# Kernel tuning notes

Measured on AMD Instinct MI355X. Metric: run time of the kernel, lower is better.

## Reference

```python
import jax, jax.numpy as jnp
import numpy as np

NUM_GRAPHS = 1024
EPS = 1e-5  # BatchNorm eps
NEG_SLOPE = 0.2  # GATConv leaky_relu slope


def _bn(x, g, b):
    # train-mode BatchNorm over node/graph axis (biased variance, as torch)
    mu = jnp.mean(x, axis=0)
    var = jnp.mean((x - mu) ** 2, axis=0)
    return (x - mu) * jax.lax.rsqrt(var + EPS) * g + b


def _prelu(x, a):
    return jnp.where(x > 0, x, a * x)


def _gat_layer(x, src, dst, W, a_src, a_dst, bias, n_nodes):
    # single-head GATConv (heads=1, concat=True), self-loops already in src/dst
    h = x @ W                                            # [N, C]
    e = jax.nn.leaky_relu(jnp.take(h @ a_src, src) + jnp.take(h @ a_dst, dst), NEG_SLOPE)  # [E]
    m = jax.ops.segment_max(e, dst, num_segments=n_nodes)
    ex = jnp.exp(e - jnp.take(m, dst))
    denom = jax.ops.segment_sum(ex, dst, num_segments=n_nodes)
    alpha = ex / (jnp.take(denom, dst) + 1e-16)          # softmax over in-edges of each target
    out = jax.ops.segment_sum(jnp.take(h, src, axis=0) * alpha[:, None], dst, num_segments=n_nodes)
    return out + bias


def setup_inputs() -> dict:
    key = jax.random.key(0)
    ks = jax.random.split(key, 16)
    N, E, F, H, C = 500_000, 8_000_000, 7, 8, 2

    def gl(k, shp, fan_in):
        return (jax.random.normal(k, shp, jnp.float32) / np.sqrt(fan_in)).astype(jnp.float32)

    return {
        "x": jax.random.normal(ks[0], (N, F), jnp.float32),
        "edge_index": jax.random.randint(ks[1], (2, E), 0, N, jnp.int32),
        "batch": jnp.sort(jax.random.randint(ks[2], (N,), 0, NUM_GRAPHS, jnp.int32)),
        "W1": gl(ks[3], (F, H), F), "as1": gl(ks[4], (H,), H), "ad1": gl(ks[5], (H,), H), "b1": jnp.zeros((H,), jnp.float32),
        "W2": gl(ks[6], (H, H), H), "as2": gl(ks[7], (H,), H), "ad2": gl(ks[8], (H,), H), "b2": jnp.zeros((H,), jnp.float32),
        "W3": gl(ks[9], (H, H), H), "as3": gl(ks[10], (H,), H), "ad3": gl(ks[11], (H,), H), "b3": jnp.zeros((H,), jnp.float32),
        "g1": jnp.ones((H,), jnp.float32), "be1": jnp.zeros((H,), jnp.float32),
        "g2": jnp.ones((H,), jnp.float32), "be2": jnp.zeros((H,), jnp.float32),
        "g3": jnp.ones((H,), jnp.float32), "be3": jnp.zeros((H,), jnp.float32),
        "a_gnn": jnp.float32(0.25),
        "Wjk": gl(ks[12], (3 * H, H), 3 * H), "bjk": jnp.zeros((H,), jnp.float32),
        "Wm1": gl(ks[13], (H, H), H), "bm1": jnp.zeros((H,), jnp.float32),
        "gm": jnp.ones((H,), jnp.float32), "bem": jnp.zeros((H,), jnp.float32),
        "a_mlp": jnp.float32(0.25),
        "Wm2": gl(ks[14], (H, C), H), "bm2": jnp.zeros((C,), jnp.float32),
    }


def reference(x, edge_index, batch,
              W1, as1, ad1, b1, W2, as2, ad2, b2, W3, as3, ad3, b3,
              g1, be1, g2, be2, g3, be3, a_gnn, Wjk, bjk,
              Wm1, bm1, gm, bem, a_mlp, Wm2, bm2):
    N = x.shape[0]
    loop = jnp.arange(N, dtype=edge_index.dtype)  # GATConv add_self_loops=True
    src = jnp.concatenate([edge_index[0], loop])
    dst = jnp.concatenate([edge_index[1], loop])
    # 3-layer GAT, each: conv -> BatchNorm -> PReLU (dropout omitted: eval)
    h1 = _prelu(_bn(_gat_layer(x, src, dst, W1, as1, ad1, b1, N), g1, be1), a_gnn)
    h2 = _prelu(_bn(_gat_layer(h1, src, dst, W2, as2, ad2, b2, N), g2, be2), a_gnn)
    h3 = _prelu(_bn(_gat_layer(h2, src, dst, W3, as3, ad3, b3, N), g3, be3), a_gnn)
    # JumpingKnowledge 'cat' + projection to out_channels
    h = jnp.concatenate([h1, h2, h3], axis=1) @ Wjk + bjk   # [N, 8]
    pooled = jax.ops.segment_sum(h, batch, num_segments=NUM_GRAPHS)  # global_add_pool [G, 8]
    m1 = _prelu(_bn(pooled @ Wm1 + bm1, gm, bem), a_mlp)    # MLP hidden
    return m1 @ Wm2 + bm2                                    # [G, 2] logits
```

## Files before the change

### kernel.cpp

```cpp
#include <hip/hip_runtime.h>

typedef unsigned short u16;
typedef unsigned int   u32;

#define EPSBN     1e-5f
#define NEG_SLOPE 0.2f
#define NGRAPH    1024
#define NPB       512
#define CHUNK     16384
#define BKCAP     11264
#define NTILE     8
#define SLOTS     1536


static __device__ __forceinline__ float bfl(const u16* __restrict__ p, int i){
    return __uint_as_float(((u32)p[i]) << 16);
}
static __device__ __forceinline__ float ldf(const void* __restrict__ p, int i, bool f32){
    return f32 ? ((const float*)p)[i] : bfl((const u16*)p, i);
}
static __device__ __forceinline__ u16 f2bf(float f){
    u32 u = __float_as_uint(f);
    return (u16)((u + 0x7fffu + ((u >> 16) & 1u)) >> 16);
}
static __device__ __forceinline__ void unpack8(uint4 pk, float* a){
    a[0] = __uint_as_float((pk.x & 0xffffu) << 16);
    a[1] = __uint_as_float( pk.x & 0xffff0000u);
    a[2] = __uint_as_float((pk.y & 0xffffu) << 16);
    a[3] = __uint_as_float( pk.y & 0xffff0000u);
    a[4] = __uint_as_float((pk.z & 0xffffu) << 16);
    a[5] = __uint_as_float( pk.z & 0xffff0000u);
    a[6] = __uint_as_float((pk.w & 0xffffu) << 16);
    a[7] = __uint_as_float( pk.w & 0xffff0000u);
}
static __device__ __forceinline__ uint4 pack8(const float* a){
    uint4 pk;
    pk.x = (u32)f2bf(a[0]) | ((u32)f2bf(a[1])<<16);
    pk.y = (u32)f2bf(a[2]) | ((u32)f2bf(a[3])<<16);
    pk.z = (u32)f2bf(a[4]) | ((u32)f2bf(a[5])<<16);
    pk.w = (u32)f2bf(a[6]) | ((u32)f2bf(a[7])<<16);
    return pk;
}

static __device__ __forceinline__ int wave_scan_incl(int x){
    int lane = threadIdx.x & 63;
    #pragma unroll
    for (int off = 1; off < 64; off <<= 1){
        int y = __shfl_up(x, off, 64);
        if (lane >= off) x += y;
    }
    return x;
}
static __device__ __forceinline__ int block_scan_incl(int x, int* wpart){
    int t = threadIdx.x, lane = t & 63, wv = t >> 6;
    int nw = blockDim.x >> 6;
    int ws = wave_scan_incl(x);
    __syncthreads();
    if (lane == 63) wpart[wv] = ws;
    __syncthreads();
    if (wv == 0){
        int p = (lane < nw) ? wpart[lane] : 0;
        p = wave_scan_incl(p);
        if (lane < nw) wpart[lane] = p;
    }
    __syncthreads();
    int base = wv ? wpart[wv-1] : 0;
    return base + ws;
}

__global__ void k_sniff(const u16* __restrict__ x, int* __restrict__ flag){
    int lane = threadIdx.x;
    bool hit = false;
    for (int i = lane; i < 128; i += 64){
        float v = bfl(x, i);
        if (!(fabsf(v) <= 1e6f)) hit = true;
    }
    unsigned long long m = __ballot(hit);
    if (lane == 0) flag[0] = (m != 0ull) ? 1 : 0;
}

__global__ __launch_bounds__(1024) void k_binsort(const int* __restrict__ src,
                                                  const int* __restrict__ dst,
                                                  u32* __restrict__ stage,
                                                  int* __restrict__ matL,
                                                  int E, int B){
    __shared__ u32 pr[CHUNK];
    __shared__ int h[2048];
    __shared__ int wpart[16];
    int c = blockIdx.x, t = threadIdx.x;
    int e0 = c << 14, e1 = min(e0 + CHUNK, E), cn = e1 - e0;
    for (int b = t; b < B; b += 1024) h[b] = 0;
    __syncthreads();
    for (int i = e0 + t; i < e1; i += 1024) atomicAdd(&h[dst[i] >> 9], 1);
    __syncthreads();
    int base = t << 1, run = 0, loc[2];
    #pragma unroll
    for (int j = 0; j < 2; j++){
        int b = base + j;
        int v = (b < B) ? h[b] : 0;
        loc[j] = run; run += v;
    }
    int incl = block_scan_incl(run, wpart);
    int bex = incl - run;
    __syncthreads();
    #pragma unroll
    for (int j = 0; j < 2; j++){
        int b = base + j;
        if (b < B) h[b] = bex + loc[j];
    }
    __syncthreads();
    int* mrow = matL + (size_t)c * (B+1);
    for (int b = t; b < B; b += 1024) mrow[b] = h[b];
    if (t == 0) mrow[B] = cn;
    __syncthreads();
    for (int i = e0 + t; i < e1; i += 1024){
        int d = dst[i];
        int b = d >> 9;
        int p = atomicAdd(&h[b], 1);
        pr[p] = ((u32)src[i] << 9) | (u32)(d & 511);
    }
    __syncthreads();
    u32* srow = stage + ((size_t)c << 14);
    for (int i = t; i < cn; i += 1024) srow[i] = pr[i];
}

__global__ __launch_bounds__(256) void k_mtrans(const int* __restrict__ matL,
                                                int* __restrict__ matT, int R, int C){
    __shared__ int tile[32][33];
    int tx = threadIdx.x & 31, ty = threadIdx.x >> 5;
    int c0 = blockIdx.x << 5, r0 = blockIdx.y << 5;
    for (int j = ty; j < 32; j += 8){
        int r = r0 + j, c = c0 + tx;
        if (r < C && c < R) tile[j][tx] = matL[(size_t)r*R + c];
    }
    __syncthreads();
    for (int j = ty; j < 32; j += 8){
        int cc = c0 + j, rr = r0 + tx;
        if (cc < R && rr < C) matT[(size_t)cc*C + rr] = tile[tx][j];
    }
}

__global__ __launch_bounds__(256) void k_bucketsum(const int* __restrict__ matT,
                                                   int* __restrict__ bb, int B, int NC){
    int b = blockIdx.x, t = threadIdx.x;
    __shared__ int s[256];
    int acc = 0;
    const int* r0 = matT + (size_t)b*NC;
    const int* r1 = matT + (size_t)(b+1)*NC;
    for (int c = t; c < NC; c += 256) acc += r1[c] - r0[c];
    s[t] = acc; __syncthreads();
    for (int off = 128; off > 0; off >>= 1){
        if (t < off) s[t] += s[t+off];
        __syncthreads();
    }
    if (t == 0) bb[b] = s[0];
}

__global__ __launch_bounds__(1024) void k_bktbase(int* __restrict__ bb, int B,
                                                  float* __restrict__ statsAll){
    __shared__ int wpart[16];
    int t = threadIdx.x;
    if (t < 48) statsAll[t] = 0.f;
    int v = (t < B) ? bb[t] : 0;
    int incl = block_scan_incl(v, wpart);
    if (t < B) bb[t] = incl - v;
    if (t == B-1) bb[B] = incl;
}

__global__ __launch_bounds__(1024) void k_bucket(const u32* __restrict__ stage,
                                                 const int* __restrict__ matT,
                                                 const int* __restrict__ bb,
                                                 int* __restrict__ tileOfs,
                                                 u32* __restrict__ csr,
                                                 int N, int B, int NC){
    __shared__ u32 pr[BKCAP];
    __shared__ int hist[4096];
    __shared__ int sc[1024];
    __shared__ int lofsA[512];
    __shared__ int wpart[16];
    int k = blockIdx.x, t = threadIdx.x;
    int n0 = k << 9, n1 = min(n0 + NPB, N), nn = n1 - n0;
    int cnt = 0, lofs = 0;
    if (t < NC){
        lofs = matT[(size_t)k*NC + t];
        cnt  = matT[(size_t)(k+1)*NC + t] - lofs;
    }
    if (t < 512) lofsA[t] = lofs;
    int incl1 = block_scan_incl(cnt, wpart);
    sc[t] = incl1;
    __syncthreads();
    int total = sc[1023];
    int ec    = min(total, BKCAP - nn);
    for (int pidx = t; pidx < ec; pidx += 1024){
        int lo = 0, hi = 511;
        while (lo < hi){ int mid = (lo + hi) >> 1; if (sc[mid] > pidx) hi = mid; else lo = mid + 1; }
        int segStart = lo ? sc[lo-1] : 0;
        pr[pidx] = stage[((size_t)lo << 14) + lofsA[lo] + (pidx - segStart)];
    }
    __syncthreads();
    for (int j = t; j < nn; j += 1024) pr[ec + j] = ((u32)(n0 + j) << 9) | (u32)j;
    int ecnt = ec + nn;
    for (int i = t; i < 4096; i += 1024) hist[i] = 0;
    __syncthreads();
    for (int i = t; i < ecnt; i += 1024){
        u32 pk = pr[i];
        int dl = pk & 511;
        int tile = min((int)(pk >> 9) >> 16, NTILE-1);
        atomicAdd(&hist[(tile << 9) + dl], 1);
    }
    __syncthreads();
    int base = t << 2, run = 0, loc[4];
    #pragma unroll
    for (int j = 0; j < 4; j++){ loc[j] = run; run += hist[base + j]; }
    int incl2 = block_scan_incl(run, wpart);
    int bex = incl2 - run;
    __syncthreads();
    #pragma unroll
    for (int j = 0; j < 4; j++) hist[base + j] = bex + loc[j];
    if ((t & 127) == 0) tileOfs[(size_t)k*9 + (t >> 7)] = bex;
    if (t == 0)         tileOfs[(size_t)k*9 + 8] = ecnt;
    __syncthreads();
    int wbase = bb[k] + n0;
    for (int i = t; i < ecnt; i += 1024){
        u32 pk = pr[i];
        int dl = pk & 511;
        int tile = min((int)(pk >> 9) >> 16, NTILE-1);
        int p = atomicAdd(&hist[(tile << 9) + dl], 1);
        csr[wbase + p] = pk;
    }
}

__global__ void k_transform(const uint4* __restrict__ actpk, const void* __restrict__ xraw,
                            const int* __restrict__ dflag, int fin,
                            const void* __restrict__ W, const void* __restrict__ adst,
                            const float* __restrict__ stats, const void* __restrict__ gamma,
                            const void* __restrict__ beta, const void* __restrict__ alpha,
                            uint4* __restrict__ hrec, float* __restrict__ hd, int n){
    const bool f32 = dflag[0] != 0;
    __shared__ float Wl[64], dl[8], scl[8], sft[8], alv;
    int t = threadIdx.x;
    if (t < 64)            Wl[t]   = (t < fin*8) ? ldf(W, t, f32) : 0.f;
    if (t >= 64 && t < 72) dl[t-64] = ldf(adst, t-64, f32);
    if (t == 80) alv = ldf(alpha, 0, f32);
    if (stats && t < 8){
        float invN = 1.f/(float)n;
        float mu  = stats[t]*invN;
        float var = fmaxf(stats[8+t]*invN - mu*mu, 0.f);
        float s   = ldf(gamma, t, f32)*rsqrtf(var + EPSBN);
        scl[t] = s; sft[t] = ldf(beta, t, f32) - mu*s;
    }
    __syncthreads();
    int i = blockIdx.x*blockDim.x + t;
    if (i >= n) return;
    float a[8];
    if (xraw){
        #pragma unroll
        for (int k=0;k<7;k++) a[k] = ldf(xraw, i*7 + k, f32);
        a[7] = 0.f;
    } else {
        unpack8(actpk[i], a);
        #pragma unroll
        for (int j=0;j<8;j++){
            float y = a[j]*scl[j] + sft[j];
            a[j] = (y > 0.f) ? y : alv*y;
        }
    }
    float h[8];
    #pragma unroll
    for (int j=0;j<8;j++){
        float acc = 0.f;
        #pragma unroll
        for (int k=0;k<8;k++) acc += a[k]*Wl[k*8+j];
        h[j] = acc;
    }
    float s2 = 0.f;
    #pragma unroll
    for (int j=0;j<8;j++) s2 += h[j]*dl[j];
    hd[i] = s2;
    hrec[i] = pack8(h);
}

__global__ __launch_bounds__(512) void k_aggregate(
        const u32* __restrict__ csr, const int* __restrict__ bb,
        const int* __restrict__ tileOfs,
        const uint4* __restrict__ hrec, const float* __restrict__ hd,
        const void* __restrict__ asrc, const int* __restrict__ dflag,
        uint4* __restrict__ act, float* __restrict__ stats, int n){
    const bool f32 = dflag[0] != 0;
    __shared__ u32 stg[5*SLOTS];
    __shared__ u16 bs[512], be[512];
    __shared__ float alS[8];
    __shared__ float sred[8][16];
    __shared__ int tofS[9];
    int k = blockIdx.x, t = threadIdx.x;
    int n0 = k << 9;
    int nn = min(NPB, n - n0);
    if (t < 8) alS[t] = ldf(asrc, t, f32);
    if (t < 9) tofS[t] = tileOfs[(size_t)k*9 + t];
    float hdv = (t < nn) ? hd[n0 + t] : 0.f;
    int e0 = bb[k] + n0;
    __syncthreads();
    float al[8];
    #pragma unroll
    for (int j = 0; j < 8; j++) al[j] = alS[j];
    float acc[8] = {0,0,0,0,0,0,0,0};
    float den = 0.f;

    int wt = 0, wc = 0;
    while (wt < NTILE && wc >= tofS[wt+1]){ wt++; if (wt < NTILE) wc = tofS[wt]; }

    u32 pkc[3]; uint4 hvc[3];
    if (wt < NTILE){
        int L = min(SLOTS, tofS[wt+1] - wc);
        #pragma unroll
        for (int j = 0; j < 3; j++) pkc[j] = csr[e0 + wc + min(t + (j << 9), L - 1)];
        #pragma unroll
        for (int j = 0; j < 3; j++) hvc[j] = hrec[pkc[j] >> 9];
    }

    while (wt < NTILE){
        int L = min(SLOTS, tofS[wt+1] - wc);
        __syncthreads();
        #pragma unroll
        for (int j = 0; j < 3; j++){
            int i = t + (j << 9);
            if (i < L){
                stg[0*SLOTS + i] = hvc[j].x;
                stg[1*SLOTS + i] = hvc[j].y;
                stg[2*SLOTS + i] = hvc[j].z;
                stg[3*SLOTS + i] = hvc[j].w;
                stg[4*SLOTS + i] = pkc[j] & 511u;
            }
        }
        bs[t] = 0; be[t] = 0;
        __syncthreads();
        int nwt = wt, nwc = wc + SLOTS;
        while (nwt < NTILE && nwc >= tofS[nwt+1]){ nwt++; if (nwt < NTILE) nwc = tofS[nwt]; }
        if (nwt < NTILE){
            int Ln = min(SLOTS, tofS[nwt+1] - nwc);
            #pragma unroll
            for (int j = 0; j < 3; j++) pkc[j] = csr[e0 + nwc + min(t + (j << 9), Ln - 1)];
            #pragma unroll
            for (int j = 0; j < 3; j++) hvc[j] = hrec[pkc[j] >> 9];
        }
        for (int i = t; i < L; i += 512){
            int dl = (int)stg[4*SLOTS + i];
            if (i == 0){
                bs[dl] = 0;
            } else {
                int dp = (int)stg[4*SLOTS + i - 1];
                if (dp != dl){ bs[dl] = (u16)i; be[dp] = (u16)i; }
            }
            if (i == L-1) be[dl] = (u16)L;
        }
        __syncthreads();
        {
            int p0 = bs[t], p1 = be[t];
            for (int p = p0; p < p1; ++p){
                uint4 hv = make_uint4(stg[0*SLOTS + p], stg[1*SLOTS + p],
                                      stg[2*SLOTS + p], stg[3*SLOTS + p]);
                float h[8]; unpack8(hv, h);
                float e = hdv;
                #pragma unroll
                for (int q = 0; q < 8; q++) e += h[q]*al[q];
                e = (e > 0.f) ? e : NEG_SLOPE*e;
                float w = __expf(e);
                den += w;
                #pragma unroll
                for (int q = 0; q < 8; q++) acc[q] += w*h[q];
            }
        }
        wt = nwt; wc = nwc;
    }

    float o[8] = {0,0,0,0,0,0,0,0};
    if (t < nn){
        float inv = 1.f/(den + 1e-16f);
        #pragma unroll
        for (int j = 0; j < 8; j++) o[j] = acc[j]*inv;
        act[n0 + t] = pack8(o);
    }
    float v[16];
    #pragma unroll
    for (int j=0;j<8;j++){ v[j]=o[j]; v[8+j]=o[j]*o[j]; }
    #pragma unroll
    for (int off=32; off>0; off>>=1){
        #pragma unroll
        for (int j=0;j<16;j++) v[j] += __shfl_down(v[j], off, 64);
    }
    int lane = t & 63, wv = t >> 6;
    if (lane == 0){
        #pragma unroll
        for (int j=0;j<16;j++) sred[wv][j] = v[j];
    }
    __syncthreads();
    if (t < 16){
        float tot = 0.f;
        #pragma unroll
        for (int w=0; w<8; w++) tot += sred[w][t];
        atomicAdd(&stats[t], tot);
    }
}

static __device__ __forceinline__ int lowerb(const int* __restrict__ a, int n, int key){
    int lo = 0, hi = n;
    while (lo < hi){ int mid = (lo + hi) >> 1; if (a[mid] < key) lo = mid + 1; else hi = mid; }
    return lo;
}

__global__ __launch_bounds__(256) void k_jkpool(
        const uint4* __restrict__ a1, const uint4* __restrict__ a2, const uint4* __restrict__ a3,
        const float* __restrict__ st1, const float* __restrict__ st2, const float* __restrict__ st3,
        const void* __restrict__ g1, const void* __restrict__ be1,
        const void* __restrict__ g2, const void* __restrict__ be2,
        const void* __restrict__ g3, const void* __restrict__ be3,
        const void* __restrict__ alpha,
        const void* __restrict__ Wjk, const void* __restrict__ bjk,
        const int* __restrict__ dflag,
        const int* __restrict__ batch, float* __restrict__ pooled, int n){
    const bool f32 = dflag[0] != 0;
    __shared__ float Wl[192], bl[8], scl[24], sft[24], alv;
    __shared__ int rng[2];
    int t = threadIdx.x, g = blockIdx.x;
    if (t < 192) Wl[t] = ldf(Wjk, t, f32);
    if (t < 8)   bl[t] = ldf(bjk, t, f32);
    if (t < 24){
        int L = t >> 3, j = t & 7;
        const float* st = (L==0)? st1 : (L==1)? st2 : st3;
        const void* gg  = (L==0)? g1  : (L==1)? g2  : g3;
        const void* bb_ = (L==0)? be1 : (L==1)? be2 : be3;
        float invN = 1.f/(float)n;
        float mu  = st[j]*invN;
        float var = fmaxf(st[8+j]*invN - mu*mu, 0.f);
        float s   = ldf(gg, j, f32)*rsqrtf(var + EPSBN);
        scl[t] = s; sft[t] = ldf(bb_, j, f32) - mu*s;
    }
    if (t == 30) alv = ldf(alpha, 0, f32);
    if (t == 0) rng[0] = lowerb(batch, n, g);
    if (t == 1) rng[1] = lowerb(batch, n, g+1);
    __syncthreads();
    int lo = rng[0], hi = rng[1];
    float pa[8] = {0,0,0,0,0,0,0,0};
    for (int i = lo + t; i < hi; i += 256){
        float c[24];
        unpack8(a1[i], c);
        unpack8(a2[i], c+8);
        unpack8(a3[i], c+16);
        #pragma unroll
        for (int k=0;k<24;k++){
            float y = c[k]*scl[k] + sft[k];
            c[k] = (y > 0.f) ? y : alv*y;
        }
        #pragma unroll
        for (int j=0;j<8;j++){
            float acc = bl[j];
            #pragma unroll
            for (int k=0;k<24;k++) acc += c[k]*Wl[k*8+j];
            pa[j] += acc;
        }
    }
    #pragma unroll
    for (int off=32; off>0; off>>=1){
        #pragma unroll
        for (int j=0;j<8;j++) pa[j] += __shfl_down(pa[j], off, 64);
    }
    __shared__ float sr[4][8];
    int lane = t & 63, wv = t >> 6;
    if (lane == 0){
        #pragma unroll
        for (int j=0;j<8;j++) sr[wv][j] = pa[j];
    }
    __syncthreads();
    if (t < 8){
        float tot = sr[0][t]+sr[1][t]+sr[2][t]+sr[3][t];
        pooled[(size_t)g*8 + t] = tot;
    }
}

__global__ __launch_bounds__(1024) void k_final(
        const float* __restrict__ pooled,
        const void* __restrict__ Wm1, const void* __restrict__ bm1,
        const void* __restrict__ gm, const void* __restrict__ bem,
        const void* __restrict__ am,
        const void* __restrict__ Wm2, const void* __restrict__ bm2,
        const int* __restrict__ dflag,
        float* __restrict__ out, int G){
    const bool f32 = dflag[0] != 0;
    int t = threadIdx.x;
    float tv[8] = {0,0,0,0,0,0,0,0};
    if (t < G){
        float r[8];
        #pragma unroll
        for (int j=0;j<8;j++) r[j] = pooled[(size_t)t*8+j];
        #pragma unroll
        for (int j=0;j<8;j++){
            float acc = ldf(bm1, j, f32);
            #pragma unroll
            for (int k=0;k<8;k++) acc += r[k]*ldf(Wm1, k*8+j, f32);
            tv[j] = acc;
        }
    }
    float v[16];
    #pragma unroll
    for (int j=0;j<8;j++){ v[j]=tv[j]; v[8+j]=tv[j]*tv[j]; }
    #pragma unroll
    for (int off=32; off>0; off>>=1){
        #pragma unroll
        for (int j=0;j<16;j++) v[j] += __shfl_down(v[j], off, 64);
    }
    __shared__ float sred[16][16];
    int lane = t & 63, wv = t >> 6;
    if (lane == 0){
        #pragma unroll
        for (int j=0;j<16;j++) sred[wv][j] = v[j];
    }
    __syncthreads();
    __shared__ float stt[16];
    if (t < 16){
        float tot = 0.f;
        #pragma unroll
        for (int w=0; w<16; w++) tot += sred[w][t];
        stt[t] = tot;
    }
    __syncthreads();
    if (t < G){
        float a = ldf(am, 0, f32);
        float invG = 1.f/(float)G;
        float m1[8];
        #pragma unroll
        for (int j=0;j<8;j++){
            float mu  = stt[j]*invG;
            float var = fmaxf(stt[8+j]*invG - mu*mu, 0.f);
            float y = (tv[j]-mu)*rsqrtf(var+EPSBN)*ldf(gm,j,f32)+ldf(bem,j,f32);
            m1[j] = (y>0.f)? y : a*y;
        }
        #pragma unroll
        for (int c=0;c<2;c++){
            float oacc = ldf(bm2, c, f32);
            #pragma unroll
            for (int k=0;k<8;k++) oacc += m1[k]*ldf(Wm2, k*2+c, f32);
            out[(size_t)t*2+c] = oacc;
        }
    }
}

extern "C" void kernel_launch(void* const* d_in, const int* in_sizes, int n_in,
                              void* d_out, int out_size, void* d_ws, size_t ws_size,
                              hipStream_t stream){
    const u16* x16   = (const u16*)d_in[0];
    const void* x    = d_in[0];
    const int* ei    = (const int*)d_in[1];
    const int* batch = (const int*)d_in[2];
    int N = in_sizes[2];
    int E = in_sizes[1] / 2;
    const int* srcA = ei;
    const int* dstA = ei + E;
    const void *W1=d_in[3],  *as1=d_in[4],  *ad1=d_in[5];
    const void *W2=d_in[7],  *as2=d_in[8],  *ad2=d_in[9];
    const void *W3=d_in[11], *as3=d_in[12], *ad3=d_in[13];
    const void *g1=d_in[15], *be1=d_in[16];
    const void *g2=d_in[17], *be2=d_in[18];
    const void *g3=d_in[19], *be3=d_in[20];
    const void *agnn=d_in[21];
    const void *Wjk=d_in[22], *bjk=d_in[23];
    const void *Wm1=d_in[24], *bm1=d_in[25];
    const void *gm =d_in[26], *bem=d_in[27];
    const void *amlp=d_in[28];
    const void *Wm2=d_in[29], *bm2=d_in[30];

    char* p = (char*)d_ws;
    auto carve = [&](size_t bytes) -> void* {
        void* r = (void*)p;
        p += (bytes + 255) & ~(size_t)255;
        return r;
    };
    size_t M = (size_t)E + (size_t)N;
    int nb512 = (N + 511)/512;
    int B  = (N + NPB - 1) / NPB;
    int NC = (E + CHUNK - 1) / CHUNK;
    int*   dflag  = (int*)  carve(256);
    int*   bb     = (int*)  carve(((size_t)B+1)*4);
    int*   tileOfs= (int*)  carve((size_t)B*9*4);
    int*   matL   = (int*)  carve((size_t)NC*(B+1)*4);
    int*   matT   = (int*)  carve((size_t)(B+1)*NC*4);
    u32*   stage  = (u32*)  carve((size_t)NC*CHUNK*4);
    u32*   csr    = (u32*)  carve(M*4);
    uint4* hrec   = (uint4*)carve((size_t)N*16);
    float* hd     = (float*)carve((size_t)N*4);
    uint4* act1   = (uint4*)carve((size_t)N*16);
    uint4* act2   = (uint4*)carve((size_t)N*16);
    uint4* act3   = (uint4*)carve((size_t)N*16);
    float* statsA = (float*)carve(256);
    float* stats1 = statsA;
    float* stats2 = statsA + 16;
    float* stats3 = statsA + 32;
    float* pooled = (float*)carve((size_t)NGRAPH*32);
    (void)ws_size; (void)n_in;

    k_sniff<<<1, 64, 0, stream>>>(x16, dflag);

    k_binsort  <<<NC, 1024, 0, stream>>>(srcA, dstA, stage, matL, E, B);
    {
        dim3 tg(((B+1) + 31)/32, (NC + 31)/32);
        k_mtrans<<<tg, 256, 0, stream>>>(matL, matT, B+1, NC);
    }
    k_bucketsum<<<B, 256, 0, stream>>>(matT, bb, B, NC);
    k_bktbase  <<<1, 1024, 0, stream>>>(bb, B, statsA);
    k_bucket   <<<B, 1024, 0, stream>>>(stage, matT, bb, tileOfs, csr, N, B, NC);

    k_transform <<<nb512, 512, 0, stream>>>(nullptr, x, dflag, 7, W1, ad1,
                                            nullptr, nullptr, nullptr, agnn, hrec, hd, N);
    k_aggregate <<<B, 512, 0, stream>>>(csr, bb, tileOfs, hrec, hd, as1, dflag, act1, stats1, N);
    k_transform <<<nb512, 512, 0, stream>>>(act1, nullptr, dflag, 8, W2, ad2,
                                            stats1, g1, be1, agnn, hrec, hd, N);
    k_aggregate <<<B, 512, 0, stream>>>(csr, bb, tileOfs, hrec, hd, as2, dflag, act2, stats2, N);
    k_transform <<<nb512, 512, 0, stream>>>(act2, nullptr, dflag, 8, W3, ad3,
                                            stats2, g2, be2, agnn, hrec, hd, N);
    k_aggregate <<<B, 512, 0, stream>>>(csr, bb, tileOfs, hrec, hd, as3, dflag, act3, stats3, N);

    k_jkpool<<<NGRAPH, 256, 0, stream>>>(act1, act2, act3, stats1, stats2, stats3,
                                         g1, be1, g2, be2, g3, be3, agnn,
                                         Wjk, bjk, dflag, batch, pooled, N);
    int G = out_size / 2;
    k_final <<<1, 1024, 0, stream>>>(pooled, Wm1, bm1, gm, bem, amlp, Wm2, bm2, dflag, (float*)d_out, G);
}
```

Measured before the change: 525.0 us.

## Compute edge attention weights per edge before staging to balance aggregate work

The attention logit, leaky-relu and exp are now computed per edge by the staging thread, using a shared-memory copy of the destination scores. The pre-weighted features and weights go to shared memory as fp32, so each per-destination thread only sums them. This moves the uneven per-node serial work onto evenly spread per-edge threads. In exchange the shared staging buffer holds 9 floats per edge, so the tile shrinks from 1536 to 1024 slots, which means more tile iterations and barriers. The exp is also evaluated on padded duplicate slots.

```diff
diff --git a/kernel.cpp b/kernel.cpp
--- a/kernel.cpp
+++ b/kernel.cpp
@@ -10,7 +10,7 @@
 #define CHUNK     16384
 #define BKCAP     11264
 #define NTILE     8
-#define SLOTS     1536
+#define SLOTS     1024
 
 
 static __device__ __forceinline__ float bfl(const u16* __restrict__ p, int i){
@@ -287,7 +287,9 @@
         const void* __restrict__ asrc, const int* __restrict__ dflag,
         uint4* __restrict__ act, float* __restrict__ stats, int n){
     const bool f32 = dflag[0] != 0;
-    __shared__ u32 stg[5*SLOTS];
+    __shared__ float stg[9*SLOTS];
+    __shared__ u16   sdl[SLOTS];
+    __shared__ float hdl[512];
     __shared__ u16 bs[512], be[512];
     __shared__ float alS[8];
     __shared__ float sred[8][16];
@@ -297,7 +299,7 @@
     int nn = min(NPB, n - n0);
     if (t < 8) alS[t] = ldf(asrc, t, f32);
     if (t < 9) tofS[t] = tileOfs[(size_t)k*9 + t];
-    float hdv = (t < nn) ? hd[n0 + t] : 0.f;
+    hdl[t] = (t < nn) ? hd[n0 + t] : 0.f;
     int e0 = bb[k] + n0;
     __syncthreads();
     float al[8];
@@ -309,27 +311,33 @@
     int wt = 0, wc = 0;
     while (wt < NTILE && wc >= tofS[wt+1]){ wt++; if (wt < NTILE) wc = tofS[wt]; }
 
-    u32 pkc[3]; uint4 hvc[3];
+    u32 pkc[2]; uint4 hvc[2];
     if (wt < NTILE){
         int L = min(SLOTS, tofS[wt+1] - wc);
         #pragma unroll
-        for (int j = 0; j < 3; j++) pkc[j] = csr[e0 + wc + min(t + (j << 9), L - 1)];
-        #pragma unroll
-        for (int j = 0; j < 3; j++) hvc[j] = hrec[pkc[j] >> 9];
+        for (int j = 0; j < 2; j++) pkc[j] = csr[e0 + wc + min(t + (j << 9), L - 1)];
+        #pragma unroll
+        for (int j = 0; j < 2; j++) hvc[j] = hrec[pkc[j] >> 9];
     }
 
     while (wt < NTILE){
         int L = min(SLOTS, tofS[wt+1] - wc);
         __syncthreads();
         #pragma unroll
-        for (int j = 0; j < 3; j++){
+        for (int j = 0; j < 2; j++){
             int i = t + (j << 9);
+            float h[8]; unpack8(hvc[j], h);
+            int dl = (int)(pkc[j] & 511u);
+            float e = hdl[dl];
+            #pragma unroll
+            for (int q = 0; q < 8; q++) e += h[q]*al[q];
+            e = (e > 0.f) ? e : NEG_SLOPE*e;
+            float w = __expf(e);
             if (i < L){
-                stg[0*SLOTS + i] = hvc[j].x;
-                stg[1*SLOTS + i] = hvc[j].y;
-                stg[2*SLOTS + i] = hvc[j].z;
-                stg[3*SLOTS + i] = hvc[j].w;
-                stg[4*SLOTS + i] = pkc[j] & 511u;
+                #pragma unroll
+                for (int q = 0; q < 8; q++) stg[q*SLOTS + i] = w*h[q];
+                stg[8*SLOTS + i] = w;
+                sdl[i] = (u16)dl;
             }
         }
         bs[t] = 0; be[t] = 0;
@@ -339,16 +347,16 @@
         if (nwt < NTILE){
             int Ln = min(SLOTS, tofS[nwt+1] - nwc);
             #pragma unroll
-            for (int j = 0; j < 3; j++) pkc[j] = csr[e0 + nwc + min(t + (j << 9), Ln - 1)];
+            for (int j = 0; j < 2; j++) pkc[j] = csr[e0 + nwc + min(t + (j << 9), Ln - 1)];
             #pragma unroll
-            for (int j = 0; j < 3; j++) hvc[j] = hrec[pkc[j] >> 9];
+            for (int j = 0; j < 2; j++) hvc[j] = hrec[pkc[j] >> 9];
         }
         for (int i = t; i < L; i += 512){
-            int dl = (int)stg[4*SLOTS + i];
+            int dl = (int)sdl[i];
             if (i == 0){
                 bs[dl] = 0;
             } else {
-                int dp = (int)stg[4*SLOTS + i - 1];
+                int dp = (int)sdl[i - 1];
                 if (dp != dl){ bs[dl] = (u16)i; be[dp] = (u16)i; }
             }
             if (i == L-1) be[dl] = (u16)L;
@@ -357,17 +365,9 @@
         {
             int p0 = bs[t], p1 = be[t];
             for (int p = p0; p < p1; ++p){
-                uint4 hv = make_uint4(stg[0*SLOTS + p], stg[1*SLOTS + p],
-                                      stg[2*SLOTS + p], stg[3*SLOTS + p]);
-                float h[8]; unpack8(hv, h);
-                float e = hdv;
                 #pragma unroll
-                for (int q = 0; q < 8; q++) e += h[q]*al[q];
-                e = (e > 0.f) ? e : NEG_SLOPE*e;
-                float w = __expf(e);
-                den += w;
-                #pragma unroll
-                for (int q = 0; q < 8; q++) acc[q] += w*h[q];
+                for (int q = 0; q < 8; q++) acc[q] += stg[q*SLOTS + p];
+                den += stg[8*SLOTS + p];
             }
         }
         wt = nwt; wc = nwc;
```

Measured after the change: 595.2 us. 1.13x slower.
